# Kernel optimization log

Hardware: AMD Instinct MI355X
Metric: run time of the kernel (lower is better)

Reference implementation:

```python
import jax, jax.numpy as jnp
import numpy as np

TEMP = 0.5
ALPHA = 1.0
BETA = 5.5
GAMMA = 5.0
N, D, C, M = 400, 512, 1000, 16000


def _normalize(x, axis=-1, eps=1e-12):
    return x / jnp.maximum(jnp.linalg.norm(x, axis=axis, keepdims=True), eps)


def _scale(x, target):
    # min-max scale x into the value range of target (global scalars)
    y = (x - x.min()) / (x.max() - x.min())
    y = y * (target.max() - target.min())
    y = y + target.min()
    return y


def setup_inputs() -> dict:
    key = jax.random.key(0)
    k1, k2, k3, k4 = jax.random.split(key, 4)
    image_features = jax.random.normal(k1, (N, D), dtype=jnp.float32)
    text_embeds = jax.random.normal(k2, (C, D), dtype=jnp.float32)
    support_feats = _normalize(jax.random.normal(k3, (D, M), dtype=jnp.float32), axis=0)
    support_labels = jax.random.randint(k4, (M,), 0, C)
    return {
        "image_features": image_features,
        "text_embeds": text_embeds,
        "support_feats": support_feats,
        "support_labels": support_labels,
    }


def reference(image_features, text_embeds, support_feats, support_labels):
    # one-hot support targets [M, C]
    support_targets = jax.nn.one_hot(support_labels, C, dtype=jnp.float32)

    # L2-normalize features (forward() normalizes both text and image features)
    text_features = _normalize(text_embeds, axis=-1).T          # [D, C]
    img = _normalize(image_features, axis=-1)                   # [N, D]

    # class distributions via temperature softmax
    train_logits = (support_feats.T @ text_features) / TEMP     # [M, C]
    test_logits = (img @ text_features) / TEMP                  # [N, C]
    train_log_dist = jax.nn.log_softmax(train_logits, axis=-1)  # log q  [M, C]
    test_log_dist = jax.nn.log_softmax(test_logits, axis=-1)    # log p  [N, C]
    test_dist = jnp.exp(test_log_dist)                          # p      [N, C]

    # KL(p_i || q_j) = sum_c p_ic log p_ic - sum_c p_ic log q_jc  -> one GEMM
    entropy_term = jnp.sum(test_dist * test_log_dist, axis=-1, keepdims=True)  # [N, 1]
    kl_divs = entropy_term - test_dist @ train_log_dist.T                      # [N, M]

    clip_logits = 100.0 * (img @ text_features)                 # [N, C]
    new_knowledge = img @ support_feats                         # [N, M]

    neg_affs = _scale(kl_divs, new_knowledge)                   # [N, M]
    affinities = -neg_affs
    kl_logits = affinities @ support_targets                    # [N, C]
    cache_logits = jnp.exp(-(BETA - BETA * new_knowledge)) @ support_targets  # [N, C]

    tipx_logits = clip_logits + kl_logits * GAMMA + cache_logits * ALPHA
    return tipx_logits
```

## Files before the change

### kernel.cpp

```cpp
#include <hip/hip_runtime.h>
#include <math.h>

#define TEMP_F   0.5f
#define ALPHA_F  1.0f
#define BETA_F   5.5f
#define GAMMA_F  5.0f
#define N_IMG    400
#define D_DIM    512
#define C_CLS    1000
#define C_PAD    1024
#define M_SUP    16000

typedef __attribute__((ext_vector_type(8))) short short8;
typedef __attribute__((ext_vector_type(4))) float f32x4;

__device__ __forceinline__ short f2bf(float f) {
    unsigned u = __float_as_uint(f);
    unsigned r = (u + 0x7fffu + ((u >> 16) & 1u)) >> 16;
    return (short)r;
}
__device__ __forceinline__ float bf2f(short s) {
    return __uint_as_float(((unsigned)(unsigned short)s) << 16);
}
__device__ __forceinline__ unsigned encf(float f) {
    unsigned u = __float_as_uint(f);
    return (u & 0x80000000u) ? ~u : (u | 0x80000000u);
}
__device__ __forceinline__ float decf(unsigned u) {
    return (u & 0x80000000u) ? __uint_as_float(u & 0x7FFFFFFFu) : __uint_as_float(~u);
}

__device__ __forceinline__ float block_reduce_sum(float v) {
    __shared__ float red[4];
    #pragma unroll
    for (int o = 32; o > 0; o >>= 1) v += __shfl_down(v, o, 64);
    int w = threadIdx.x >> 6, l = threadIdx.x & 63;
    __syncthreads();
    if (l == 0) red[w] = v;
    __syncthreads();
    float r = red[0];
    int nw = blockDim.x >> 6;
    for (int i = 1; i < nw; ++i) r += red[i];
    return r;
}

__device__ __forceinline__ float block_reduce_max(float v) {
    __shared__ float redm[4];
    #pragma unroll
    for (int o = 32; o > 0; o >>= 1) v = fmaxf(v, __shfl_down(v, o, 64));
    int w = threadIdx.x >> 6, l = threadIdx.x & 63;
    __syncthreads();
    if (l == 0) redm[w] = v;
    __syncthreads();
    float r = redm[0];
    int nw = blockDim.x >> 6;
    for (int i = 1; i < nw; ++i) r = fmaxf(r, redm[i]);
    return r;
}

__device__ __forceinline__ void gload_lds16(const void* g, void* l) {
    __builtin_amdgcn_global_load_lds(
        (const __attribute__((address_space(1))) unsigned int*)g,
        (__attribute__((address_space(3))) unsigned int*)l, 16, 0, 0);
}

__global__ void init_mm_k(unsigned* mm) {
    mm[0] = encf(INFINITY);
    mm[1] = encf(-INFINITY);
    mm[2] = encf(INFINITY);
    mm[3] = encf(-INFINITY);
}

__global__ void normalize_rows_k(const float* __restrict__ src, short* __restrict__ dst) {
    int row = blockIdx.x;
    const float* s = src + (long)row * D_DIM;
    short* d = dst + (long)row * D_DIM;
    float ss = 0.f;
    for (int c = threadIdx.x; c < D_DIM; c += blockDim.x) { float v = s[c]; ss += v * v; }
    float tot = block_reduce_sum(ss);
    float inv = 1.0f / fmaxf(sqrtf(tot), 1e-12f);
    for (int c = threadIdx.x; c < D_DIM; c += blockDim.x) d[c] = f2bf(s[c] * inv);
}

__global__ void transpose_bf16_k(const float* __restrict__ S, short* __restrict__ Sb) {
    __shared__ float tile[32][33];
    int m0 = blockIdx.x * 32, d0 = blockIdx.y * 32;
    int tx = threadIdx.x & 31, ty = threadIdx.x >> 5;
    #pragma unroll
    for (int r = 0; r < 32; r += 8)
        tile[ty + r][tx] = S[(long)(d0 + ty + r) * M_SUP + m0 + tx];
    __syncthreads();
    #pragma unroll
    for (int r = 0; r < 32; r += 8)
        Sb[(long)(m0 + ty + r) * D_DIM + d0 + tx] = f2bf(tile[tx][ty + r]);
}

template<int EPI, int SWZ>
__global__ __launch_bounds__(256) void mfma_gemm(
    const short* __restrict__ A, const short* __restrict__ B, void* __restrict__ Cm,
    int I, int Jclamp, int Jout, int K, long lda, long ldb, long ldc, float alpha,
    const float* __restrict__ ent, const float* __restrict__ lse, unsigned* __restrict__ mm,
    float* __restrict__ out2)
{
    __shared__ short As[3][128 * 32];
    __shared__ short Bs[3][128 * 32];
    const int tid = threadIdx.x;
    const int wave = tid >> 6;
    const int lane = tid & 63;

    int i0, j0;
    if (SWZ) {
        int lin = blockIdx.x;
        int xcd = lin & 7;
        int idx = lin >> 3;
        i0 = (idx & 3) * 128;
        j0 = (xcd * 16 + (idx >> 2)) * 128;
    } else {
        i0 = blockIdx.y * 128;
        j0 = blockIdx.x * 128;
    }

    const int srow = wave * 16 + (lane >> 2);
    const int skk  = (lane & 3) * 8;

    const int wm = (wave & 1) * 64;
    const int wn = (wave >> 1) * 64;
    const int fr = lane & 15;
    const int fq = lane >> 4;

    f32x4 acc[4][4] = {};

    auto stage = [&](int buf, int k0) {
        #pragma unroll
        for (int q = 0; q < 2; ++q) {
            int gi = i0 + q * 64 + srow; if (gi > I - 1) gi = I - 1;
            gload_lds16(A + (long)gi * lda + k0 + skk, As[buf] + q * 2048 + wave * 512);
        }
        #pragma unroll
        for (int q = 0; q < 2; ++q) {
            int gj = j0 + q * 64 + srow; if (gj > Jclamp - 1) gj = Jclamp - 1;
            gload_lds16(B + (long)gj * ldb + k0 + skk, Bs[buf] + q * 2048 + wave * 512);
        }
    };

    const int nt = K >> 5;
    stage(0, 0);
    if (nt > 1) stage(1, 32);
    if (nt > 2) stage(2, 64);

    for (int t = 0; t < nt; ++t) {
        const int b = t % 3;
        const short* Ab = &As[b][0];
        const short* Bb = &Bs[b][0];

        if (t + 2 < nt)      asm volatile("s_waitcnt vmcnt(8)" ::: "memory");
        else if (t + 1 < nt) asm volatile("s_waitcnt vmcnt(4)" ::: "memory");
        else                 asm volatile("s_waitcnt vmcnt(0)" ::: "memory");
        __builtin_amdgcn_s_barrier();
        __builtin_amdgcn_sched_barrier(0);

        short8 af[4], bfr[4];
        #pragma unroll
        for (int mi = 0; mi < 4; ++mi)
            af[mi] = *(const short8*)(Ab + (wm + mi * 16 + fr) * 32 + fq * 8);
        #pragma unroll
        for (int ni = 0; ni < 4; ++ni)
            bfr[ni] = *(const short8*)(Bb + (wn + ni * 16 + fr) * 32 + fq * 8);

        asm volatile("s_waitcnt lgkmcnt(0)" ::: "memory");
        __builtin_amdgcn_sched_barrier(0);
        __builtin_amdgcn_s_barrier();

        if (t + 3 < nt) stage(b, (t + 3) << 5);

        __builtin_amdgcn_s_setprio(1);
        #pragma unroll
        for (int mi = 0; mi < 4; ++mi)
            #pragma unroll
            for (int ni = 0; ni < 4; ++ni)
                acc[mi][ni] = __builtin_amdgcn_mfma_f32_16x16x32_bf16(
                    af[mi], bfr[ni], acc[mi][ni], 0, 0, 0);
        __builtin_amdgcn_s_setprio(0);
    }

    float lmin = INFINITY, lmax = -INFINITY;

    #pragma unroll
    for (int mi = 0; mi < 4; ++mi) {
        #pragma unroll
        for (int ni = 0; ni < 4; ++ni) {
            int gj = j0 + wn + ni * 16 + fr;
            float lsev = 0.f;
            if (EPI == 2) lsev = lse[gj < Jout ? gj : (Jout - 1)];
            #pragma unroll
            for (int t = 0; t < 4; ++t) {
                int gi = i0 + wm + mi * 16 + fq * 4 + t;
                float v = alpha * acc[mi][ni][t];
                if (EPI == 2) {
                    int gic = gi < I ? gi : (I - 1);
                    v = ent[gic] - v + lsev;
                }
                if (EPI == 2 || EPI == 3) { lmin = fminf(lmin, v); lmax = fmaxf(lmax, v); }
                if (gi < I && gj < Jout) {
                    if (EPI == 1) ((short*)Cm)[(long)gi * ldc + gj] = f2bf(v);
                    else          ((float*)Cm)[(long)gi * ldc + gj] = v;
                }
                if (EPI == 4 && gi < I && gj < C_CLS)
                    out2[(long)gi * C_CLS + gj] = 100.f * v;
            }
        }
    }

    if (EPI == 2 || EPI == 3) {
        #pragma unroll
        for (int o = 32; o > 0; o >>= 1) {
            lmin = fminf(lmin, __shfl_down(lmin, o, 64));
            lmax = fmaxf(lmax, __shfl_down(lmax, o, 64));
        }
        __shared__ float rmin[4], rmax[4];
        if (lane == 0) { rmin[wave] = lmin; rmax[wave] = lmax; }
        __syncthreads();
        if (tid == 0) {
            float bmin = fminf(fminf(rmin[0], rmin[1]), fminf(rmin[2], rmin[3]));
            float bmax = fmaxf(fmaxf(rmax[0], rmax[1]), fmaxf(rmax[2], rmax[3]));
            int base = (EPI == 2) ? 0 : 2;
            atomicMin(&mm[base + 0], encf(bmin));
            atomicMax(&mm[base + 1], encf(bmax));
        }
    }
}

__global__ void row_lse_k(const short* __restrict__ t, float* __restrict__ lse) {
    int row = blockIdx.x;
    const short* r = t + (long)row * C_PAD;
    float f[8];
    bool act = threadIdx.x < 125;
    float mx = -INFINITY;
    if (act) {
        short8 v = *(const short8*)(r + threadIdx.x * 8);
        #pragma unroll
        for (int j = 0; j < 8; ++j) { f[j] = bf2f(v[j]); mx = fmaxf(mx, f[j]); }
    }
    mx = block_reduce_max(mx);
    float se = 0.f;
    if (act) {
        #pragma unroll
        for (int j = 0; j < 8; ++j) se += __expf(f[j] - mx);
    }
    se = block_reduce_sum(se);
    if (threadIdx.x == 0) lse[row] = mx + __logf(se);
}

__global__ void test_softmax_k(const float* __restrict__ dot, short* __restrict__ p,
                               float* __restrict__ ent) {
    int n = blockIdx.x;
    const float* dr = dot + (long)n * C_PAD;
    short* pr = p + (long)n * C_PAD;
    float mx = -INFINITY;
    for (int c = threadIdx.x; c < C_CLS; c += blockDim.x) mx = fmaxf(mx, 2.f * dr[c]);
    mx = block_reduce_max(mx);
    float se = 0.f;
    for (int c = threadIdx.x; c < C_CLS; c += blockDim.x) se += __expf(2.f * dr[c] - mx);
    se = block_reduce_sum(se);
    float logsum = mx + __logf(se);
    float e = 0.f;
    for (int c = threadIdx.x; c < C_PAD; c += blockDim.x) {
        if (c < C_CLS) {
            float lp = 2.f * dr[c] - logsum;
            float pv = __expf(lp);
            pr[c] = f2bf(pv);
            e += pv * lp;
        } else {
            pr[c] = 0;
        }
    }
    e = block_reduce_sum(e);
    if (threadIdx.x == 0) ent[n] = e;
}

__global__ __launch_bounds__(256) void final_partial_k(
    const float* __restrict__ kl, const float* __restrict__ nk,
    const int* __restrict__ labels, const unsigned* __restrict__ mm,
    float* __restrict__ out)
{
    int n = blockIdx.x;
    int q = blockIdx.y;
    __shared__ float bins[C_CLS];
    for (int c = threadIdx.x; c < C_CLS; c += 256) bins[c] = 0.f;
    __syncthreads();
    float klmin = decf(mm[0]), klmax = decf(mm[1]);
    float nkmin = decf(mm[2]), nkmax = decf(mm[3]);
    float ratio = (nkmax - nkmin) / (klmax - klmin);
    const int m0 = q * (M_SUP / 4);
    const float4* kl4 = (const float4*)(kl + (long)n * M_SUP + m0);
    const float4* nk4 = (const float4*)(nk + (long)n * M_SUP + m0);
    const int4*  lb4 = (const int4*)(labels + m0);
    const int nv = M_SUP / 4 / 4;
    for (int v = threadIdx.x; v < nv; v += 256) {
        float4 kv = kl4[v];
        float4 vv = nk4[v];
        int4   lv = lb4[v];
        float y, contrib;
        y = (kv.x - klmin) * ratio + nkmin;
        contrib = -GAMMA_F * y + ALPHA_F * __expf(BETA_F * (vv.x - 1.0f));
        atomicAdd(&bins[lv.x], contrib);
        y = (kv.y - klmin) * ratio + nkmin;
        contrib = -GAMMA_F * y + ALPHA_F * __expf(BETA_F * (vv.y - 1.0f));
        atomicAdd(&bins[lv.y], contrib);
        y = (kv.z - klmin) * ratio + nkmin;
        contrib = -GAMMA_F * y + ALPHA_F * __expf(BETA_F * (vv.z - 1.0f));
        atomicAdd(&bins[lv.z], contrib);
        y = (kv.w - klmin) * ratio + nkmin;
        contrib = -GAMMA_F * y + ALPHA_F * __expf(BETA_F * (vv.w - 1.0f));
        atomicAdd(&bins[lv.w], contrib);
    }
    __syncthreads();
    for (int c = threadIdx.x; c < C_CLS; c += 256)
        atomicAdd(&out[(long)n * C_CLS + c], bins[c]);
}

extern "C" void kernel_launch(void* const* d_in, const int* in_sizes, int n_in,
                              void* d_out, int out_size, void* d_ws, size_t ws_size,
                              hipStream_t stream) {
    const float* image_features = (const float*)d_in[0];
    const float* text_embeds    = (const float*)d_in[1];
    const float* support_feats  = (const float*)d_in[2];
    const int*   support_labels = (const int*)d_in[3];
    float* out = (float*)d_out;

    char* base = (char*)d_ws;
    size_t off = 0;
    auto alloc = [&](size_t bytes) {
        void* p = base + off;
        off = (off + bytes + 255) & ~(size_t)255;
        return p;
    };
    short* Tnb  = (short*)alloc(sizeof(short) * C_CLS * D_DIM);
    short* imgb = (short*)alloc(sizeof(short) * N_IMG * D_DIM);
    short* Sb   = (short*)alloc(sizeof(short) * M_SUP * D_DIM);
    short* tb   = (short*)alloc(sizeof(short) * M_SUP * C_PAD);
    short* pb   = (short*)alloc(sizeof(short) * N_IMG * C_PAD);
    float* dot  = (float*)alloc(sizeof(float) * N_IMG * C_PAD);
    float* lse  = (float*)alloc(sizeof(float) * M_SUP);
    float* ent  = (float*)alloc(sizeof(float) * N_IMG);
    float* kl   = (float*)alloc(sizeof(float) * N_IMG * M_SUP);
    float* nk   = (float*)alloc(sizeof(float) * N_IMG * M_SUP);
    unsigned* mm = (unsigned*)alloc(256);

    init_mm_k<<<1, 1, 0, stream>>>(mm);
    normalize_rows_k<<<C_CLS, 256, 0, stream>>>(text_embeds, Tnb);
    normalize_rows_k<<<N_IMG, 256, 0, stream>>>(image_features, imgb);
    transpose_bf16_k<<<dim3(M_SUP / 32, D_DIM / 32), 256, 0, stream>>>(support_feats, Sb);

    mfma_gemm<1, 0><<<dim3(8, 125), 256, 0, stream>>>(
        Sb, Tnb, tb, M_SUP, C_CLS, C_PAD, D_DIM, D_DIM, D_DIM, C_PAD, 2.0f,
        nullptr, nullptr, nullptr, nullptr);

    row_lse_k<<<M_SUP, 128, 0, stream>>>(tb, lse);

    mfma_gemm<4, 0><<<dim3(8, 4), 256, 0, stream>>>(
        imgb, Tnb, dot, N_IMG, C_CLS, C_PAD, D_DIM, D_DIM, D_DIM, C_PAD, 1.0f,
        nullptr, nullptr, nullptr, out);

    test_softmax_k<<<N_IMG, 256, 0, stream>>>(dot, pb, ent);

    mfma_gemm<2, 1><<<512, 256, 0, stream>>>(
        pb, tb, kl, N_IMG, M_SUP, M_SUP, C_PAD, C_PAD, C_PAD, M_SUP, 1.0f,
        ent, lse, mm, nullptr);

    mfma_gemm<3, 1><<<512, 256, 0, stream>>>(
        imgb, Sb, nk, M_SUP > 0 ? N_IMG : N_IMG, M_SUP, M_SUP, D_DIM, D_DIM, D_DIM, M_SUP, 1.0f,
        nullptr, nullptr, mm, nullptr);

    final_partial_k<<<dim3(N_IMG, 4), 256, 0, stream>>>(kl, nk, support_labels, mm, out);
}
```

Baseline: 247.8 us.

## Fuse KL and support GEMMs, vectorize transpose and softmax kernels, add XCD swizzle

```diff
diff --git a/kernel.cpp b/kernel.cpp
--- a/kernel.cpp
+++ b/kernel.cpp
@@ -12,6 +12,7 @@
 #define M_SUP    16000
 
 typedef __attribute__((ext_vector_type(8))) short short8;
+typedef __attribute__((ext_vector_type(4))) short short4v;
 typedef __attribute__((ext_vector_type(4))) float f32x4;
 
 __device__ __forceinline__ short f2bf(float f) {
@@ -44,24 +45,85 @@
     return r;
 }
 
-__device__ __forceinline__ float block_reduce_max(float v) {
-    __shared__ float redm[4];
-    #pragma unroll
-    for (int o = 32; o > 0; o >>= 1) v = fmaxf(v, __shfl_down(v, o, 64));
-    int w = threadIdx.x >> 6, l = threadIdx.x & 63;
-    __syncthreads();
-    if (l == 0) redm[w] = v;
-    __syncthreads();
-    float r = redm[0];
-    int nw = blockDim.x >> 6;
-    for (int i = 1; i < nw; ++i) r = fmaxf(r, redm[i]);
-    return r;
-}
-
 __device__ __forceinline__ void gload_lds16(const void* g, void* l) {
     __builtin_amdgcn_global_load_lds(
         (const __attribute__((address_space(1))) unsigned int*)g,
         (__attribute__((address_space(3))) unsigned int*)l, 16, 0, 0);
+}
+
+__device__ __forceinline__ void stage_tile(
+    const short* __restrict__ A, const short* __restrict__ B,
+    int I, int Jclamp, int i0, int j0, long lda, long ldb,
+    short* Asb, short* Bsb, int wave, int lane, int k0)
+{
+    const int srow = wave * 16 + (lane >> 2);
+    const int skk  = (lane & 3) * 8;
+    #pragma unroll
+    for (int q = 0; q < 2; ++q) {
+        int gi = i0 + q * 64 + srow; if (gi > I - 1) gi = I - 1;
+        gload_lds16(A + (long)gi * lda + k0 + skk, Asb + q * 2048 + wave * 512);
+    }
+    #pragma unroll
+    for (int q = 0; q < 2; ++q) {
+        int gj = j0 + q * 64 + srow; if (gj > Jclamp - 1) gj = Jclamp - 1;
+        gload_lds16(B + (long)gj * ldb + k0 + skk, Bsb + q * 2048 + wave * 512);
+    }
+}
+
+template<bool PRESTAGED>
+__device__ __forceinline__ void gemm_pipe(
+    const short* __restrict__ A, const short* __restrict__ B,
+    int I, int Jclamp, int i0, int j0, int K, long lda, long ldb,
+    short (*As)[4096], short (*Bs)[4096], int wave, int lane,
+    f32x4 acc[4][4])
+{
+    const int wm = (wave & 1) * 64;
+    const int wn = (wave >> 1) * 64;
+    const int fr = lane & 15;
+    const int fq = lane >> 4;
+    const int nt = K >> 5;
+
+    if (!PRESTAGED) {
+        stage_tile(A, B, I, Jclamp, i0, j0, lda, ldb, As[0], Bs[0], wave, lane, 0);
+        if (nt > 1) stage_tile(A, B, I, Jclamp, i0, j0, lda, ldb, As[1], Bs[1], wave, lane, 32);
+        if (nt > 2) stage_tile(A, B, I, Jclamp, i0, j0, lda, ldb, As[2], Bs[2], wave, lane, 64);
+    }
+
+    for (int t = 0; t < nt; ++t) {
+        const int b = t % 3;
+        const short* Ab = &As[b][0];
+        const short* Bb = &Bs[b][0];
+
+        if (t + 2 < nt)      asm volatile("s_waitcnt vmcnt(8)" ::: "memory");
+        else if (t + 1 < nt) asm volatile("s_waitcnt vmcnt(4)" ::: "memory");
+        else                 asm volatile("s_waitcnt vmcnt(0)" ::: "memory");
+        __builtin_amdgcn_s_barrier();
+        __builtin_amdgcn_sched_barrier(0);
+
+        short8 af[4], bfr[4];
+        #pragma unroll
+        for (int mi = 0; mi < 4; ++mi)
+            af[mi] = *(const short8*)(Ab + (wm + mi * 16 + fr) * 32 + fq * 8);
+        #pragma unroll
+        for (int ni = 0; ni < 4; ++ni)
+            bfr[ni] = *(const short8*)(Bb + (wn + ni * 16 + fr) * 32 + fq * 8);
+
+        asm volatile("s_waitcnt lgkmcnt(0)" ::: "memory");
+        __builtin_amdgcn_sched_barrier(0);
+        __builtin_amdgcn_s_barrier();
+
+        if (t + 3 < nt)
+            stage_tile(A, B, I, Jclamp, i0, j0, lda, ldb, As[b], Bs[b], wave, lane, (t + 3) << 5);
+
+        __builtin_amdgcn_s_setprio(1);
+        #pragma unroll
+        for (int mi = 0; mi < 4; ++mi)
+            #pragma unroll
+            for (int ni = 0; ni < 4; ++ni)
+                acc[mi][ni] = __builtin_amdgcn_mfma_f32_16x16x32_bf16(
+                    af[mi], bfr[ni], acc[mi][ni], 0, 0, 0);
+        __builtin_amdgcn_s_setprio(0);
+    }
 }
 
 __global__ void init_mm_k(unsigned* mm) {
@@ -83,45 +145,52 @@
 }
 
 __global__ void transpose_bf16_k(const float* __restrict__ S, short* __restrict__ Sb) {
-    __shared__ float tile[32][33];
-    int m0 = blockIdx.x * 32, d0 = blockIdx.y * 32;
-    int tx = threadIdx.x & 31, ty = threadIdx.x >> 5;
-    #pragma unroll
-    for (int r = 0; r < 32; r += 8)
-        tile[ty + r][tx] = S[(long)(d0 + ty + r) * M_SUP + m0 + tx];
+    __shared__ float tile[64][65];
+    int m0 = blockIdx.x * 64, d0 = blockIdx.y * 64;
+    int ml = (threadIdx.x & 15) * 4;
+    int dl = threadIdx.x >> 4;
+    #pragma unroll
+    for (int r = 0; r < 64; r += 16) {
+        f32x4 v = *(const f32x4*)(S + (long)(d0 + dl + r) * M_SUP + m0 + ml);
+        tile[dl + r][ml + 0] = v[0];
+        tile[dl + r][ml + 1] = v[1];
+        tile[dl + r][ml + 2] = v[2];
+        tile[dl + r][ml + 3] = v[3];
+    }
     __syncthreads();
-    #pragma unroll
-    for (int r = 0; r < 32; r += 8)
-        Sb[(long)(m0 + ty + r) * D_DIM + d0 + tx] = f2bf(tile[tx][ty + r]);
+    int mw = threadIdx.x >> 4;
+    int dc = (threadIdx.x & 15) * 4;
+    #pragma unroll
+    for (int r = 0; r < 64; r += 16) {
+        short4v o;
+        #pragma unroll
+        for (int k = 0; k < 4; ++k) o[k] = f2bf(tile[dc + k][mw + r]);
+        *(short4v*)(Sb + (long)(m0 + mw + r) * D_DIM + d0 + dc) = o;
+    }
 }
 
 template<int EPI, int SWZ>
 __global__ __launch_bounds__(256) void mfma_gemm(
     const short* __restrict__ A, const short* __restrict__ B, void* __restrict__ Cm,
     int I, int Jclamp, int Jout, int K, long lda, long ldb, long ldc, float alpha,
-    const float* __restrict__ ent, const float* __restrict__ lse, unsigned* __restrict__ mm,
     float* __restrict__ out2)
 {
-    __shared__ short As[3][128 * 32];
-    __shared__ short Bs[3][128 * 32];
+    __shared__ short As[3][4096];
+    __shared__ short Bs[3][4096];
     const int tid = threadIdx.x;
     const int wave = tid >> 6;
     const int lane = tid & 63;
 
     int i0, j0;
-    if (SWZ) {
+    if (SWZ == 2) {
         int lin = blockIdx.x;
-        int xcd = lin & 7;
-        int idx = lin >> 3;
-        i0 = (idx & 3) * 128;
-        j0 = (xcd * 16 + (idx >> 2)) * 128;
+        int gt = (lin & 7) * 125 + (lin >> 3);
+        i0 = (gt >> 3) * 128;
+        j0 = (gt & 7) * 128;
     } else {
         i0 = blockIdx.y * 128;
         j0 = blockIdx.x * 128;
     }
-
-    const int srow = wave * 16 + (lane >> 2);
-    const int skk  = (lane & 3) * 8;
 
     const int wm = (wave & 1) * 64;
     const int wn = (wave >> 1) * 64;
@@ -129,78 +198,17 @@
     const int fq = lane >> 4;
 
     f32x4 acc[4][4] = {};
-
-    auto stage = [&](int buf, int k0) {
-        #pragma unroll
-        for (int q = 0; q < 2; ++q) {
-            int gi = i0 + q * 64 + srow; if (gi > I - 1) gi = I - 1;
-            gload_lds16(A + (long)gi * lda + k0 + skk, As[buf] + q * 2048 + wave * 512);
-        }
-        #pragma unroll
-        for (int q = 0; q < 2; ++q) {
-            int gj = j0 + q * 64 + srow; if (gj > Jclamp - 1) gj = Jclamp - 1;
-            gload_lds16(B + (long)gj * ldb + k0 + skk, Bs[buf] + q * 2048 + wave * 512);
-        }
-    };
-
-    const int nt = K >> 5;
-    stage(0, 0);
-    if (nt > 1) stage(1, 32);
-    if (nt > 2) stage(2, 64);
-
-    for (int t = 0; t < nt; ++t) {
-        const int b = t % 3;
-        const short* Ab = &As[b][0];
-        const short* Bb = &Bs[b][0];
-
-        if (t + 2 < nt)      asm volatile("s_waitcnt vmcnt(8)" ::: "memory");
-        else if (t + 1 < nt) asm volatile("s_waitcnt vmcnt(4)" ::: "memory");
-        else                 asm volatile("s_waitcnt vmcnt(0)" ::: "memory");
-        __builtin_amdgcn_s_barrier();
-        __builtin_amdgcn_sched_barrier(0);
-
-        short8 af[4], bfr[4];
-        #pragma unroll
-        for (int mi = 0; mi < 4; ++mi)
-            af[mi] = *(const short8*)(Ab + (wm + mi * 16 + fr) * 32 + fq * 8);
-        #pragma unroll
-        for (int ni = 0; ni < 4; ++ni)
-            bfr[ni] = *(const short8*)(Bb + (wn + ni * 16 + fr) * 32 + fq * 8);
-
-        asm volatile("s_waitcnt lgkmcnt(0)" ::: "memory");
-        __builtin_amdgcn_sched_barrier(0);
-        __builtin_amdgcn_s_barrier();
-
-        if (t + 3 < nt) stage(b, (t + 3) << 5);
-
-        __builtin_amdgcn_s_setprio(1);
-        #pragma unroll
-        for (int mi = 0; mi < 4; ++mi)
-            #pragma unroll
-            for (int ni = 0; ni < 4; ++ni)
-                acc[mi][ni] = __builtin_amdgcn_mfma_f32_16x16x32_bf16(
-                    af[mi], bfr[ni], acc[mi][ni], 0, 0, 0);
-        __builtin_amdgcn_s_setprio(0);
-    }
-
-    float lmin = INFINITY, lmax = -INFINITY;
+    gemm_pipe<false>(A, B, I, Jclamp, i0, j0, K, lda, ldb, As, Bs, wave, lane, acc);
 
     #pragma unroll
     for (int mi = 0; mi < 4; ++mi) {
         #pragma unroll
         for (int ni = 0; ni < 4; ++ni) {
             int gj = j0 + wn + ni * 16 + fr;
-            float lsev = 0.f;
-            if (EPI == 2) lsev = lse[gj < Jout ? gj : (Jout - 1)];
             #pragma unroll
             for (int t = 0; t < 4; ++t) {
                 int gi = i0 + wm + mi * 16 + fq * 4 + t;
                 float v = alpha * acc[mi][ni][t];
-                if (EPI == 2) {
-                    int gic = gi < I ? gi : (I - 1);
-                    v = ent[gic] - v + lsev;
-                }
-                if (EPI == 2 || EPI == 3) { lmin = fminf(lmin, v); lmax = fmaxf(lmax, v); }
                 if (gi < I && gj < Jout) {
                     if (EPI == 1) ((short*)Cm)[(long)gi * ldc + gj] = f2bf(v);
                     else          ((float*)Cm)[(long)gi * ldc + gj] = v;
@@ -210,72 +218,190 @@
             }
         }
     }
-
-    if (EPI == 2 || EPI == 3) {
+}
+
+__global__ __launch_bounds__(256) void gemm23_k(
+    const short* __restrict__ imgb, const short* __restrict__ Sb,
+    const short* __restrict__ pb, const short* __restrict__ tb,
+    float* __restrict__ nk, float* __restrict__ kl,
+    const float* __restrict__ ent, const float* __restrict__ lse,
+    unsigned* __restrict__ mm)
+{
+    __shared__ short As[3][4096];
+    __shared__ short Bs[3][4096];
+    const int tid = threadIdx.x;
+    const int wave = tid >> 6;
+    const int lane = tid & 63;
+
+    int lin = blockIdx.x;
+    int xcd = lin & 7;
+    int idx = lin >> 3;
+    int i0 = (idx & 3) * 128;
+    int j0 = (xcd * 16 + (idx >> 2)) * 128;
+
+    const int wm = (wave & 1) * 64;
+    const int wn = (wave >> 1) * 64;
+    const int fr = lane & 15;
+    const int fq = lane >> 4;
+
+    f32x4 acc[4][4] = {};
+
+    gemm_pipe<false>(imgb, Sb, N_IMG, M_SUP, i0, j0, D_DIM, D_DIM, D_DIM,
+                     As, Bs, wave, lane, acc);
+
+    stage_tile(pb, tb, N_IMG, M_SUP, i0, j0, C_PAD, C_PAD, As[0], Bs[0], wave, lane, 0);
+    stage_tile(pb, tb, N_IMG, M_SUP, i0, j0, C_PAD, C_PAD, As[1], Bs[1], wave, lane, 32);
+    stage_tile(pb, tb, N_IMG, M_SUP, i0, j0, C_PAD, C_PAD, As[2], Bs[2], wave, lane, 64);
+
+    {
+        float lmin = INFINITY, lmax = -INFINITY;
+        #pragma unroll
+        for (int mi = 0; mi < 4; ++mi) {
+            #pragma unroll
+            for (int ni = 0; ni < 4; ++ni) {
+                int gj = j0 + wn + ni * 16 + fr;
+                #pragma unroll
+                for (int t = 0; t < 4; ++t) {
+                    int gi = i0 + wm + mi * 16 + fq * 4 + t;
+                    float v = acc[mi][ni][t];
+                    lmin = fminf(lmin, v); lmax = fmaxf(lmax, v);
+                    if (gi < N_IMG && gj < M_SUP)
+                        nk[(long)gi * M_SUP + gj] = v;
+                }
+            }
+        }
         #pragma unroll
         for (int o = 32; o > 0; o >>= 1) {
             lmin = fminf(lmin, __shfl_down(lmin, o, 64));
             lmax = fmaxf(lmax, __shfl_down(lmax, o, 64));
         }
-        __shared__ float rmin[4], rmax[4];
-        if (lane == 0) { rmin[wave] = lmin; rmax[wave] = lmax; }
-        __syncthreads();
-        if (tid == 0) {
-            float bmin = fminf(fminf(rmin[0], rmin[1]), fminf(rmin[2], rmin[3]));
-            float bmax = fmaxf(fmaxf(rmax[0], rmax[1]), fmaxf(rmax[2], rmax[3]));
-            int base = (EPI == 2) ? 0 : 2;
-            atomicMin(&mm[base + 0], encf(bmin));
-            atomicMax(&mm[base + 1], encf(bmax));
+        if (lane == 0) {
+            atomicMin(&mm[2], encf(lmin));
+            atomicMax(&mm[3], encf(lmax));
+        }
+    }
+
+    #pragma unroll
+    for (int mi = 0; mi < 4; ++mi)
+        #pragma unroll
+        for (int ni = 0; ni < 4; ++ni)
+            acc[mi][ni] = (f32x4){0.f, 0.f, 0.f, 0.f};
+
+    gemm_pipe<true>(pb, tb, N_IMG, M_SUP, i0, j0, C_PAD, C_PAD, C_PAD,
+                    As, Bs, wave, lane, acc);
+
+    {
+        float lmin = INFINITY, lmax = -INFINITY;
+        #pragma unroll
+        for (int mi = 0; mi < 4; ++mi) {
+            #pragma unroll
+            for (int ni = 0; ni < 4; ++ni) {
+                int gj = j0 + wn + ni * 16 + fr;
+                float lsev = lse[gj < M_SUP ? gj : (M_SUP - 1)];
+                #pragma unroll
+                for (int t = 0; t < 4; ++t) {
+                    int gi = i0 + wm + mi * 16 + fq * 4 + t;
+                    int gic = gi < N_IMG ? gi : (N_IMG - 1);
+                    float v = ent[gic] - acc[mi][ni][t] + lsev;
+                    lmin = fminf(lmin, v); lmax = fmaxf(lmax, v);
+                    if (gi < N_IMG && gj < M_SUP)
+                        kl[(long)gi * M_SUP + gj] = v;
+                }
+            }
+        }
+        #pragma unroll
+        for (int o = 32; o > 0; o >>= 1) {
+            lmin = fminf(lmin, __shfl_down(lmin, o, 64));
+            lmax = fmaxf(lmax, __shfl_down(lmax, o, 64));
+        }
+        if (lane == 0) {
+            atomicMin(&mm[0], encf(lmin));
+            atomicMax(&mm[1], encf(lmax));
         }
     }
 }
 
 __global__ void row_lse_k(const short* __restrict__ t, float* __restrict__ lse) {
-    int row = blockIdx.x;
+    int row = blockIdx.x * 4 + (threadIdx.x >> 6);
+    int lane = threadIdx.x & 63;
     const short* r = t + (long)row * C_PAD;
-    float f[8];
-    bool act = threadIdx.x < 125;
+    short8 v0 = *(const short8*)(r + lane * 8);
+    short8 v1 = *(const short8*)(r + 512 + lane * 8);
+    bool act1 = lane < 61;
+    float f0[8], f1[8];
     float mx = -INFINITY;
-    if (act) {
-        short8 v = *(const short8*)(r + threadIdx.x * 8);
-        #pragma unroll
-        for (int j = 0; j < 8; ++j) { f[j] = bf2f(v[j]); mx = fmaxf(mx, f[j]); }
-    }
-    mx = block_reduce_max(mx);
+    #pragma unroll
+    for (int j = 0; j < 8; ++j) { f0[j] = bf2f(v0[j]); mx = fmaxf(mx, f0[j]); }
+    if (act1) {
+        #pragma unroll
+        for (int j = 0; j < 8; ++j) { f1[j] = bf2f(v1[j]); mx = fmaxf(mx, f1[j]); }
+    }
+    #pragma unroll
+    for (int o = 32; o > 0; o >>= 1) mx = fmaxf(mx, __shfl_xor(mx, o, 64));
     float se = 0.f;
-    if (act) {
-        #pragma unroll
-        for (int j = 0; j < 8; ++j) se += __expf(f[j] - mx);
-    }
-    se = block_reduce_sum(se);
-    if (threadIdx.x == 0) lse[row] = mx + __logf(se);
+    #pragma unroll
+    for (int j = 0; j < 8; ++j) se += __expf(f0[j] - mx);
+    if (act1) {
+        #pragma unroll
+        for (int j = 0; j < 8; ++j) se += __expf(f1[j] - mx);
+    }
+    #pragma unroll
+    for (int o = 32; o > 0; o >>= 1) se += __shfl_xor(se, o, 64);
+    if (lane == 0) lse[row] = mx + __logf(se);
 }
 
 __global__ void test_softmax_k(const float* __restrict__ dot, short* __restrict__ p,
                                float* __restrict__ ent) {
-    int n = blockIdx.x;
+    int n = blockIdx.x * 4 + (threadIdx.x >> 6);
+    int lane = threadIdx.x & 63;
     const float* dr = dot + (long)n * C_PAD;
     short* pr = p + (long)n * C_PAD;
+    f32x4 v[4];
+    #pragma unroll
+    for (int pp = 0; pp < 4; ++pp)
+        v[pp] = *(const f32x4*)(dr + pp * 256 + lane * 4);
     float mx = -INFINITY;
-    for (int c = threadIdx.x; c < C_CLS; c += blockDim.x) mx = fmaxf(mx, 2.f * dr[c]);
-    mx = block_reduce_max(mx);
+    #pragma unroll
+    for (int pp = 0; pp < 4; ++pp) {
+        bool valid = (pp < 3) || (lane < 58);
+        if (valid)
+            #pragma unroll
+            for (int j = 0; j < 4; ++j) mx = fmaxf(mx, 2.f * v[pp][j]);
+    }
+    #pragma unroll
+    for (int o = 32; o > 0; o >>= 1) mx = fmaxf(mx, __shfl_xor(mx, o, 64));
     float se = 0.f;
-    for (int c = threadIdx.x; c < C_CLS; c += blockDim.x) se += __expf(2.f * dr[c] - mx);
-    se = block_reduce_sum(se);
+    #pragma unroll
+    for (int pp = 0; pp < 4; ++pp) {
+        bool valid = (pp < 3) || (lane < 58);
+        if (valid)
+            #pragma unroll
+            for (int j = 0; j < 4; ++j) se += __expf(2.f * v[pp][j] - mx);
+    }
+    #pragma unroll
+    for (int o = 32; o > 0; o >>= 1) se += __shfl_xor(se, o, 64);
     float logsum = mx + __logf(se);
     float e = 0.f;
-    for (int c = threadIdx.x; c < C_PAD; c += blockDim.x) {
-        if (c < C_CLS) {
-            float lp = 2.f * dr[c] - logsum;
-            float pv = __expf(lp);
-            pr[c] = f2bf(pv);
-            e += pv * lp;
-        } else {
-            pr[c] = 0;
-        }
-    }
-    e = block_reduce_sum(e);
-    if (threadIdx.x == 0) ent[n] = e;
+    #pragma unroll
+    for (int pp = 0; pp < 4; ++pp) {
+        bool valid = (pp < 3) || (lane < 58);
+        short4v o4;
+        #pragma unroll
+        for (int j = 0; j < 4; ++j) {
+            if (valid) {
+                float lp = 2.f * v[pp][j] - logsum;
+                float pv = __expf(lp);
+                o4[j] = f2bf(pv);
+                e += pv * lp;
+            } else {
+                o4[j] = 0;
+            }
+        }
+        *(short4v*)(pr + pp * 256 + lane * 4) = o4;
+    }
+    #pragma unroll
+    for (int o = 32; o > 0; o >>= 1) e += __shfl_xor(e, o, 64);
+    if (lane == 0) ent[n] = e;
 }
 
 __global__ __launch_bounds__(256) void final_partial_k(
@@ -350,27 +476,19 @@
     init_mm_k<<<1, 1, 0, stream>>>(mm);
     normalize_rows_k<<<C_CLS, 256, 0, stream>>>(text_embeds, Tnb);
     normalize_rows_k<<<N_IMG, 256, 0, stream>>>(image_features, imgb);
-    transpose_bf16_k<<<dim3(M_SUP / 32, D_DIM / 32), 256, 0, stream>>>(support_feats, Sb);
-
-    mfma_gemm<1, 0><<<dim3(8, 125), 256, 0, stream>>>(
-        Sb, Tnb, tb, M_SUP, C_CLS, C_PAD, D_DIM, D_DIM, D_DIM, C_PAD, 2.0f,
-        nullptr, nullptr, nullptr, nullptr);
-
-    row_lse_k<<<M_SUP, 128, 0, stream>>>(tb, lse);
+    transpose_bf16_k<<<dim3(M_SUP / 64, D_DIM / 64), 256, 0, stream>>>(support_feats, Sb);
 
     mfma_gemm<4, 0><<<dim3(8, 4), 256, 0, stream>>>(
-        imgb, Tnb, dot, N_IMG, C_CLS, C_PAD, D_DIM, D_DIM, D_DIM, C_PAD, 1.0f,
-        nullptr, nullptr, nullptr, out);
-
-    test_softmax_k<<<N_IMG, 256, 0, stream>>>(dot, pb, ent);
-
-    mfma_gemm<2, 1><<<512, 256, 0, stream>>>(
-        pb, tb, kl, N_IMG, M_SUP, M_SUP, C_PAD, C_PAD, C_PAD, M_SUP, 1.0f,
-        ent, lse, mm, nullptr);
-
-    mfma_gemm<3, 1><<<512, 256, 0, stream>>>(
-        imgb, Sb, nk, M_SUP > 0 ? N_IMG : N_IMG, M_SUP, M_SUP, D_DIM, D_DIM, D_DIM, M_SUP, 1.0f,
-        nullptr, nullptr, mm, nullptr);
+        imgb, Tnb, dot, N_IMG, C_CLS, C_PAD, D_DIM, D_DIM, D_DIM, C_PAD, 1.0f, out);
+
+    test_softmax_k<<<N_IMG / 4, 256, 0, stream>>>(dot, pb, ent);
+
+    mfma_gemm<1, 2><<<1000, 256, 0, stream>>>(
+        Sb, Tnb, tb, M_SUP, C_CLS, C_PAD, D_DIM, D_DIM, D_DIM, C_PAD, 2.0f, nullptr);
+
+    row_lse_k<<<M_SUP / 4, 256, 0, stream>>>(tb, lse);
+
+    gemm23_k<<<512, 256, 0, stream>>>(imgb, Sb, pb, tb, nk, kl, ent, lse, mm);
 
     final_partial_k<<<dim3(N_IMG, 4), 256, 0, stream>>>(kl, nk, support_labels, mm, out);
 }
```

Result: slower. 292.7 us (+18.1%).
